# Kernel optimization log

Hardware: AMD Instinct MI355X
Metric: run time of the kernel (lower is better)

## Reference

```python
import jax, jax.numpy as jnp
import numpy as np

N = 50000      # nodes
E = 800000     # directed edges (avg degree 16)
IN, HID, OUT = 256, 128, 16


def setup_inputs() -> dict:
    key = jax.random.key(0)
    ks = jax.random.split(key, 8)
    x = jax.random.normal(ks[0], (N, IN), dtype=jnp.float32)
    edge_index = jax.random.randint(ks[1], (2, E), 0, N)
    W1 = jax.random.normal(ks[2], (IN, HID), dtype=jnp.float32) * (1.0 / np.sqrt(IN))
    b1 = jnp.zeros((HID,), jnp.float32)
    W2 = jax.random.normal(ks[3], (HID, HID), dtype=jnp.float32) * (1.0 / np.sqrt(HID))
    b2 = jnp.zeros((HID,), jnp.float32)
    Wc = jax.random.normal(ks[4], (HID, OUT), dtype=jnp.float32) * (1.0 / np.sqrt(HID))
    bc = jnp.zeros((OUT,), jnp.float32)
    return {"x": x, "W1": W1, "b1": b1, "W2": W2, "b2": b2,
            "Wc": Wc, "bc": bc, "edge_index": edge_index, "conv_time": 30}


def _gcn_norm(edge_index, n, dtype):
    # add self-loops, compute symmetric GCN normalization D^{-1/2}(A+I)D^{-1/2}
    loops = jnp.arange(n)
    src = jnp.concatenate([edge_index[0], loops])
    dst = jnp.concatenate([edge_index[1], loops])
    deg = jax.ops.segment_sum(jnp.ones_like(dst, dtype=dtype), dst, num_segments=n)
    dinv = jnp.where(deg > 0, jax.lax.rsqrt(deg), jnp.zeros_like(deg))
    norm = dinv[src] * dinv[dst]          # [E+N] edge weights
    return src, dst, norm


def _propagate(h, src, dst, norm, n, hops):
    # hops is a static Python int (conv_time)
    for _ in range(hops):
        h = jax.ops.segment_sum(h[src] * norm[:, None], dst, num_segments=n)
    return h


def reference(x, W1, b1, W2, b2, Wc, bc, edge_index, conv_time):
    n = x.shape[0]
    src, dst, norm = _gcn_norm(edge_index, n, x.dtype)
    # conv1: linear only (conv_time = 0)
    h = jax.nn.relu(x @ W1 + b1)
    # dropout is identity in eval mode
    # conv2: linear + conv_time hops of normalized propagation
    h = _propagate(h @ W2 + b2, src, dst, norm, n, int(conv_time))
    h = jax.nn.relu(h)
    # cls: linear + 1 hop
    h = _propagate(h @ Wc + bc, src, dst, norm, n, 1)
    return h
```

## Files before the change

### kernel.cpp

```cpp
#include <hip/hip_runtime.h>
#include <hip/hip_fp16.h>

#define NNODES 50000
#define NEDGES 800000
#define IN_F   256
#define HID_F  128
#define OUT_F  16
#define HOPS   30
#define MPAD   50048

typedef unsigned int u32;
typedef unsigned long long u64;
typedef _Float16 f16;
typedef f16 f16x8 __attribute__((ext_vector_type(8)));
typedef float f32x4 __attribute__((ext_vector_type(4)));
typedef u32 u32x4 __attribute__((ext_vector_type(4)));

union U32H2 { u32 u; __half2 h; };

__device__ inline float2 upk(u32 v) {
    U32H2 t; t.u = v;
    return __half22float2(t.h);
}
__device__ inline u32 pk2(float a, float b) {
    U32H2 t; t.h = __floats2half2_rn(a, b);
    return t.u;
}


__global__ void k_init_deg(int* __restrict__ deg, int n) {
    int i = blockIdx.x * blockDim.x + threadIdx.x;
    if (i < n) deg[i] = 1;
}

__global__ void k_count(const int* __restrict__ dst, int* __restrict__ deg, int e) {
    int i = blockIdx.x * blockDim.x + threadIdx.x;
    if (i < e) atomicAdd(&deg[dst[i]], 1);
}

__global__ void k_dinv(const int* __restrict__ deg, float* __restrict__ dinv, int n) {
    int i = blockIdx.x * blockDim.x + threadIdx.x;
    if (i < n) dinv[i] = rsqrtf((float)deg[i]);
}

__global__ void k_scan1(const int* __restrict__ deg, int* __restrict__ bsums, int n) {
    __shared__ int sh[256];
    int tid = threadIdx.x;
    int i = blockIdx.x * 256 + tid;
    sh[tid] = (i < n) ? deg[i] : 0;
    __syncthreads();
    for (int ofs = 128; ofs > 0; ofs >>= 1) {
        if (tid < ofs) sh[tid] += sh[tid + ofs];
        __syncthreads();
    }
    if (tid == 0) bsums[blockIdx.x] = sh[0];
}

__global__ void k_scan2(int* __restrict__ bsums, int nb, int* __restrict__ rp, int n) {
    if (threadIdx.x == 0 && blockIdx.x == 0) {
        int run = 0;
        for (int b = 0; b < nb; ++b) { int t = bsums[b]; bsums[b] = run; run += t; }
        rp[n] = run;
    }
}

__global__ void k_scan3(const int* __restrict__ deg, const int* __restrict__ bsums,
                        int* __restrict__ rp, int* __restrict__ cursor, int n) {
    __shared__ int sh[256];
    int tid = threadIdx.x;
    int i = blockIdx.x * 256 + tid;
    int v = (i < n) ? deg[i] : 0;
    sh[tid] = v;
    __syncthreads();
    for (int ofs = 1; ofs < 256; ofs <<= 1) {
        int t = 0;
        if (tid >= ofs) t = sh[tid - ofs];
        __syncthreads();
        sh[tid] += t;
        __syncthreads();
    }
    if (i < n) {
        int excl = sh[tid] - v + bsums[blockIdx.x];
        rp[i] = excl;
        cursor[i] = excl;
    }
}

__global__ void k_scatter(const int* __restrict__ src, const int* __restrict__ dst,
                          const float* __restrict__ dinv, int* __restrict__ cursor,
                          int2* __restrict__ ew, int e, int n) {
    int t = blockIdx.x * blockDim.x + threadIdx.x;
    if (t < e) {
        int s = src[t], d = dst[t];
        int pos = atomicAdd(&cursor[d], 1);
        ew[pos] = make_int2(s, __float_as_int(dinv[s] * dinv[d]));
    } else if (t < e + n) {
        int i = t - e;
        int pos = atomicAdd(&cursor[i], 1);
        float di = dinv[i];
        ew[pos] = make_int2(i, __float_as_int(di * di));
    }
}

__global__ void k_sortwave(const int* __restrict__ rp, int2* __restrict__ ew, int n) {
    int node = blockIdx.x * 4 + (threadIdx.x >> 6);
    int lane = threadIdx.x & 63;
    if (node >= n) return;
    int beg = rp[node], end = rp[node + 1];
    int deg = end - beg;
    if (deg > 64) return;
    int2 my = make_int2(0x7fffffff, 0);
    if (lane < deg) my = ew[beg + lane];
    int rank = 0;
    for (int k = 0; k < deg; ++k) {
        int sk = __shfl(my.x, k);
        rank += (sk < my.x) || (sk == my.x && k < lane);
    }
    if (lane < deg) ew[beg + rank] = my;
}

template<int K, int NC>
__global__ void k_cast_wt(const float* __restrict__ W, f16* __restrict__ Wt) {
    int i = blockIdx.x * blockDim.x + threadIdx.x;
    if (i < K * NC) {
        int k = i / NC, c = i % NC;
        Wt[(size_t)c * K + k] = (f16)W[i];
    }
}


template<int K, bool RELU, typename TA>
__global__ __launch_bounds__(256)
void k_gemm_mfma(const TA* __restrict__ A, const f16* __restrict__ Wt,
                 const float* __restrict__ b, f16* __restrict__ C, int M) {
    constexpr int KC = (K > 128) ? 128 : K;
    __shared__ f16 sa[64][KC + 8];
    __shared__ f16 sb[128][KC + 8];
    int tid  = threadIdx.x;
    int wid  = tid >> 6;
    int lane = tid & 63;
    int row0 = blockIdx.x * 64;
    int rowW = row0 + wid * 16;
    int rl   = lane & 15;
    int kc   = (lane >> 4) * 8;

    f32x4 acc[8];
#pragma unroll
    for (int n = 0; n < 8; ++n) acc[n] = (f32x4)0.f;

    int lr = wid * 16 + rl;

    for (int c = 0; c < K / KC; ++c) {
        int k0 = c * KC;
        if (c > 0) __syncthreads();
        if constexpr (sizeof(TA) == 4) {
            const float4* A4 = reinterpret_cast<const float4*>(A);
            constexpr int C4 = KC / 4;
            for (int idx = tid; idx < 64 * C4; idx += 256) {
                int r  = idx / C4;
                int c4 = idx % C4;
                int gr = row0 + r;
                if (gr >= M) gr = M - 1;
                float4 v = A4[(size_t)gr * (K / 4) + k0 / 4 + c4];
                f16 o[4] = {(f16)v.x, (f16)v.y, (f16)v.z, (f16)v.w};
                *reinterpret_cast<u64*>(&sa[r][c4 * 4]) = *reinterpret_cast<u64*>(o);
            }
        } else {
            const u32x4* A4 = reinterpret_cast<const u32x4*>(A);
            constexpr int C8 = KC / 8;
            for (int idx = tid; idx < 64 * C8; idx += 256) {
                int r  = idx / C8;
                int c8 = idx % C8;
                int gr = row0 + r;
                if (gr >= M) gr = M - 1;
                u32x4 v = A4[(size_t)gr * (K / 8) + k0 / 8 + c8];
                *reinterpret_cast<u32x4*>(&sa[r][c8 * 8]) = v;
            }
        }
        {
            const u32x4* B4 = reinterpret_cast<const u32x4*>(Wt);
            constexpr int C8 = KC / 8;
            for (int idx = tid; idx < 128 * C8; idx += 256) {
                int r  = idx / C8;
                int c8 = idx % C8;
                u32x4 v = B4[(size_t)r * (K / 8) + k0 / 8 + c8];
                *reinterpret_cast<u32x4*>(&sb[r][c8 * 8]) = v;
            }
        }
        __syncthreads();

#pragma unroll
        for (int kk = 0; kk < KC; kk += 32) {
            f16x8 aF = *reinterpret_cast<const f16x8*>(&sa[lr][kk + kc]);
#pragma unroll
            for (int n = 0; n < 8; ++n) {
                f16x8 bF = *reinterpret_cast<const f16x8*>(&sb[n * 16 + rl][kk + kc]);
                acc[n] = __builtin_amdgcn_mfma_f32_16x16x32_f16(aF, bF, acc[n], 0, 0, 0);
            }
        }
    }

#pragma unroll
    for (int n = 0; n < 8; ++n) {
        int col = n * 16 + rl;
        float bias = b[col];
#pragma unroll
        for (int j = 0; j < 4; ++j) {
            int row = rowW + 4 * (lane >> 4) + j;
            if (row < M) {
                float s = acc[n][j] + bias;
                if (RELU) s = fmaxf(s, 0.f);
                C[(size_t)row * 128 + col] = (f16)s;
            }
        }
    }
}


template<bool RELU>
__global__ void k_proph(const u32* __restrict__ Hin, u32* __restrict__ Hout,
                        const int* __restrict__ rp, const int2* __restrict__ ew,
                        int n) {
    int grp  = threadIdx.x >> 4;
    int lane = threadIdx.x & 15;
    int node = blockIdx.x * 16 + grp;
    if (node >= n) return;
    int beg = rp[node], end = rp[node + 1];
    const u32x4* H4 = reinterpret_cast<const u32x4*>(Hin);

    float acc[8];
#pragma unroll
    for (int i = 0; i < 8; ++i) acc[i] = 0.f;

    auto body = [&](int e) {
        int2 p   = ew[e];
        float ww = __int_as_float(p.y);
        u32x4 v  = H4[(size_t)p.x * 16 + lane];
#pragma unroll
        for (int q = 0; q < 4; ++q) {
            float2 f = upk(v[q]);
            acc[q * 2 + 0] += ww * f.x;
            acc[q * 2 + 1] += ww * f.y;
        }
    };

    int e = beg;
    for (; e + 1 < end; e += 2) { body(e); body(e + 1); }
    if (e < end) body(e);

    if (RELU) {
#pragma unroll
        for (int i = 0; i < 8; ++i) acc[i] = fmaxf(acc[i], 0.f);
    }
    u32x4 o;
#pragma unroll
    for (int q = 0; q < 4; ++q) o[q] = pk2(acc[q * 2], acc[q * 2 + 1]);
    reinterpret_cast<u32x4*>(Hout)[(size_t)node * 16 + lane] = o;
}


__global__ void k_cls_h(const u32* __restrict__ Ah, const float* __restrict__ Wc,
                        const float* __restrict__ bc, float* __restrict__ G, int M) {
    __shared__ float sa[64][132];
    __shared__ float4 sw4[512];
    int tid  = threadIdx.x;
    int row0 = blockIdx.x * 64;

    for (int idx = tid; idx < 512; idx += 256)
        sw4[idx] = reinterpret_cast<const float4*>(Wc)[idx];

    const uint4* A4 = reinterpret_cast<const uint4*>(Ah);
    for (int idx = tid; idx < 64 * 16; idx += 256) {
        int r = idx >> 4, c = idx & 15;
        int gr = row0 + r;
        uint4 v = (gr < M) ? A4[(size_t)gr * 16 + c]
                           : make_uint4(0u, 0u, 0u, 0u);
        float* dst = &sa[r][c * 8];
        const u32* vv = reinterpret_cast<const u32*>(&v);
#pragma unroll
        for (int q = 0; q < 4; ++q) {
            float2 f = upk(vv[q]);
            dst[q * 2 + 0] = f.x;
            dst[q * 2 + 1] = f.y;
        }
    }
    __syncthreads();

    int tc = tid & 3;
    int tr = tid >> 2;
    float4 acc = make_float4(0.f, 0.f, 0.f, 0.f);
    for (int k4 = 0; k4 < 32; ++k4) {
        float4 a = *reinterpret_cast<const float4*>(&sa[tr][k4 * 4]);
        const float* af = reinterpret_cast<const float*>(&a);
#pragma unroll
        for (int kk = 0; kk < 4; ++kk) {
            float4 wv = sw4[(k4 * 4 + kk) * 4 + tc];
            float av = af[kk];
            acc.x += av * wv.x; acc.y += av * wv.y;
            acc.z += av * wv.z; acc.w += av * wv.w;
        }
    }
    int r = row0 + tr;
    if (r < M) {
        float4 bb = reinterpret_cast<const float4*>(bc)[tc];
        acc.x += bb.x; acc.y += bb.y; acc.z += bb.z; acc.w += bb.w;
        reinterpret_cast<float4*>(G)[(size_t)r * 4 + tc] = acc;
    }
}


__global__ void k_prop16(const float* __restrict__ Gin, float* __restrict__ Out,
                         const int* __restrict__ rp, const int2* __restrict__ ew,
                         int n) {
    int g    = blockIdx.x * 64 + (threadIdx.x >> 2);
    int lane = threadIdx.x & 3;
    if (g >= n) return;
    int beg = rp[g], end = rp[g + 1];
    const float4* G4 = reinterpret_cast<const float4*>(Gin);
    float ax = 0.f, ay = 0.f, az = 0.f, aw = 0.f;
    for (int e = beg; e < end; ++e) {
        int2 p   = ew[e];
        float ww = __int_as_float(p.y);
        float4 hv = G4[(size_t)p.x * 4 + lane];
        ax += ww * hv.x; ay += ww * hv.y; az += ww * hv.z; aw += ww * hv.w;
    }
    reinterpret_cast<float4*>(Out)[(size_t)g * 4 + lane] = make_float4(ax, ay, az, aw);
}


extern "C" void kernel_launch(void* const* d_in, const int* in_sizes, int n_in,
                              void* d_out, int out_size, void* d_ws, size_t ws_size,
                              hipStream_t stream) {
    const float* x  = (const float*)d_in[0];
    const float* W1 = (const float*)d_in[1];
    const float* b1 = (const float*)d_in[2];
    const float* W2 = (const float*)d_in[3];
    const float* b2 = (const float*)d_in[4];
    const float* Wc = (const float*)d_in[5];
    const float* bc = (const float*)d_in[6];
    const int*   ei = (const int*)d_in[7];
    const int* srcp = ei;
    const int* dstp = ei + NEDGES;
    float* out = (float*)d_out;

    char* p = (char*)d_ws;
    auto alloc = [&](size_t bytes) -> char* {
        char* r = p;
        p += (bytes + 255) & ~(size_t)255;
        return r;
    };
    int*   deg    = (int*)  alloc(NNODES * 4);
    float* dinv   = (float*)alloc(NNODES * 4);
    int*   rp     = (int*)  alloc((NNODES + 1) * 4);
    int*   cursor = (int*)  alloc(NNODES * 4);
    int*   bsums  = (int*)  alloc(256 * 4);
    int2*  ew     = (int2*) alloc((size_t)(NEDGES + NNODES) * 8);
    f16*   W1t    = (f16*)  alloc((size_t)HID_F * IN_F * 2);
    f16*   W2t    = (f16*)  alloc((size_t)HID_F * HID_F * 2);
    f16*   H0h    = (f16*)  alloc((size_t)MPAD * HID_F * 2);
    u32*   Hh0    = (u32*)  alloc((size_t)MPAD * HID_F * 2);
    u32*   Hh1    = (u32*)  alloc((size_t)NNODES * HID_F * 2);
    float* G      = (float*)alloc((size_t)NNODES * OUT_F * 4);

    const int T = 256;
    auto nb = [](int n, int t) { return (n + t - 1) / t; };

    k_init_deg<<<nb(NNODES, T), T, 0, stream>>>(deg, NNODES);
    k_count<<<nb(NEDGES, T), T, 0, stream>>>(dstp, deg, NEDGES);
    k_dinv<<<nb(NNODES, T), T, 0, stream>>>(deg, dinv, NNODES);
    int NB = nb(NNODES, 256);
    k_scan1<<<NB, 256, 0, stream>>>(deg, bsums, NNODES);
    k_scan2<<<1, 1, 0, stream>>>(bsums, NB, rp, NNODES);
    k_scan3<<<NB, 256, 0, stream>>>(deg, bsums, rp, cursor, NNODES);
    k_scatter<<<nb(NEDGES + NNODES, T), T, 0, stream>>>(srcp, dstp, dinv, cursor,
                                                        ew, NEDGES, NNODES);
    k_sortwave<<<nb(NNODES, 4), 256, 0, stream>>>(rp, ew, NNODES);

    k_cast_wt<IN_F,  HID_F><<<nb(IN_F * HID_F, T), T, 0, stream>>>(W1, W1t);
    k_cast_wt<HID_F, HID_F><<<nb(HID_F * HID_F, T), T, 0, stream>>>(W2, W2t);

    int GB = MPAD / 64;
    k_gemm_mfma<IN_F,  true,  float><<<GB, 256, 0, stream>>>(x,   W1t, b1, H0h, NNODES);
    k_gemm_mfma<HID_F, false, f16  ><<<GB, 256, 0, stream>>>(H0h, W2t, b2, (f16*)Hh0, NNODES);

    u32* cur = Hh0;
    u32* nxt = Hh1;
    int PB = nb(NNODES, 16);
    for (int i = 0; i < HOPS; ++i) {
        if (i == HOPS - 1)
            k_proph<true ><<<PB, 256, 0, stream>>>(cur, nxt, rp, ew, NNODES);
        else
            k_proph<false><<<PB, 256, 0, stream>>>(cur, nxt, rp, ew, NNODES);
        u32* t = cur; cur = nxt; nxt = t;
    }

    k_cls_h<<<nb(NNODES, 64), 256, 0, stream>>>(cur, Wc, bc, G, NNODES);
    k_prop16<<<nb(NNODES, 64), 256, 0, stream>>>(G, out, rp, ew, NNODES);
}
```

Before: 1.076 ms.

## Fuse GEMMs with edge scatter and sort into shared launches

Merges the first GEMM with the CSR edge scatter, and the second GEMM with the per-node edge sort, into single kernels that split work by block index. The GEMM tile shrinks its K chunk to 64, issues all global loads into registers before writing shared memory, and sets a launch-bounds occupancy hint. The aim is to overlap independent preprocessing with GEMM work and cut launch count. In exchange, the heterogeneous blocks may compete for resources and the smaller K chunk adds more synchronisation steps.

Result: faster. 1.053 ms (-2.1%).

```diff
diff --git a/kernel.cpp b/kernel.cpp
--- a/kernel.cpp
+++ b/kernel.cpp
@@ -8,6 +8,7 @@
 #define OUT_F  16
 #define HOPS   30
 #define MPAD   50048
+#define GB_GEMM (MPAD / 64)
 
 typedef unsigned int u32;
 typedef unsigned long long u64;
@@ -86,39 +87,6 @@
     }
 }
 
-__global__ void k_scatter(const int* __restrict__ src, const int* __restrict__ dst,
-                          const float* __restrict__ dinv, int* __restrict__ cursor,
-                          int2* __restrict__ ew, int e, int n) {
-    int t = blockIdx.x * blockDim.x + threadIdx.x;
-    if (t < e) {
-        int s = src[t], d = dst[t];
-        int pos = atomicAdd(&cursor[d], 1);
-        ew[pos] = make_int2(s, __float_as_int(dinv[s] * dinv[d]));
-    } else if (t < e + n) {
-        int i = t - e;
-        int pos = atomicAdd(&cursor[i], 1);
-        float di = dinv[i];
-        ew[pos] = make_int2(i, __float_as_int(di * di));
-    }
-}
-
-__global__ void k_sortwave(const int* __restrict__ rp, int2* __restrict__ ew, int n) {
-    int node = blockIdx.x * 4 + (threadIdx.x >> 6);
-    int lane = threadIdx.x & 63;
-    if (node >= n) return;
-    int beg = rp[node], end = rp[node + 1];
-    int deg = end - beg;
-    if (deg > 64) return;
-    int2 my = make_int2(0x7fffffff, 0);
-    if (lane < deg) my = ew[beg + lane];
-    int rank = 0;
-    for (int k = 0; k < deg; ++k) {
-        int sk = __shfl(my.x, k);
-        rank += (sk < my.x) || (sk == my.x && k < lane);
-    }
-    if (lane < deg) ew[beg + rank] = my;
-}
-
 template<int K, int NC>
 __global__ void k_cast_wt(const float* __restrict__ W, f16* __restrict__ Wt) {
     int i = blockIdx.x * blockDim.x + threadIdx.x;
@@ -130,16 +98,16 @@
 
 
 template<int K, bool RELU, typename TA>
-__global__ __launch_bounds__(256)
-void k_gemm_mfma(const TA* __restrict__ A, const f16* __restrict__ Wt,
-                 const float* __restrict__ b, f16* __restrict__ C, int M) {
-    constexpr int KC = (K > 128) ? 128 : K;
+__device__ void gemm_tile(const TA* __restrict__ A, const f16* __restrict__ Wt,
+                          const float* __restrict__ b, f16* __restrict__ C,
+                          int M, int bid) {
+    constexpr int KC = 64;
     __shared__ f16 sa[64][KC + 8];
     __shared__ f16 sb[128][KC + 8];
     int tid  = threadIdx.x;
     int wid  = tid >> 6;
     int lane = tid & 63;
-    int row0 = blockIdx.x * 64;
+    int row0 = bid * 64;
     int rowW = row0 + wid * 16;
     int rl   = lane & 15;
     int kc   = (lane >> 4) * 8;
@@ -149,42 +117,71 @@
     for (int n = 0; n < 8; ++n) acc[n] = (f32x4)0.f;
 
     int lr = wid * 16 + rl;
+    const u32x4* B4 = reinterpret_cast<const u32x4*>(Wt);
 
     for (int c = 0; c < K / KC; ++c) {
         int k0 = c * KC;
         if (c > 0) __syncthreads();
         if constexpr (sizeof(TA) == 4) {
             const float4* A4 = reinterpret_cast<const float4*>(A);
-            constexpr int C4 = KC / 4;
-            for (int idx = tid; idx < 64 * C4; idx += 256) {
-                int r  = idx / C4;
-                int c4 = idx % C4;
+            float4 av[4];
+            u32x4  bv[4];
+#pragma unroll
+            for (int j = 0; j < 4; ++j) {
+                int idx = tid + j * 256;
+                int r = idx >> 4, c4 = idx & 15;
                 int gr = row0 + r;
                 if (gr >= M) gr = M - 1;
-                float4 v = A4[(size_t)gr * (K / 4) + k0 / 4 + c4];
-                f16 o[4] = {(f16)v.x, (f16)v.y, (f16)v.z, (f16)v.w};
+                av[j] = A4[(size_t)gr * (K / 4) + k0 / 4 + c4];
+            }
+#pragma unroll
+            for (int j = 0; j < 4; ++j) {
+                int idx = tid + j * 256;
+                int r = idx >> 3, c8 = idx & 7;
+                bv[j] = B4[(size_t)r * (K / 8) + k0 / 8 + c8];
+            }
+#pragma unroll
+            for (int j = 0; j < 4; ++j) {
+                int idx = tid + j * 256;
+                int r = idx >> 4, c4 = idx & 15;
+                f16 o[4] = {(f16)av[j].x, (f16)av[j].y, (f16)av[j].z, (f16)av[j].w};
                 *reinterpret_cast<u64*>(&sa[r][c4 * 4]) = *reinterpret_cast<u64*>(o);
+            }
+#pragma unroll
+            for (int j = 0; j < 4; ++j) {
+                int idx = tid + j * 256;
+                int r = idx >> 3, c8 = idx & 7;
+                *reinterpret_cast<u32x4*>(&sb[r][c8 * 8]) = bv[j];
             }
         } else {
             const u32x4* A4 = reinterpret_cast<const u32x4*>(A);
-            constexpr int C8 = KC / 8;
-            for (int idx = tid; idx < 64 * C8; idx += 256) {
-                int r  = idx / C8;
-                int c8 = idx % C8;
+            u32x4 av[2];
+            u32x4 bv[4];
+#pragma unroll
+            for (int j = 0; j < 2; ++j) {
+                int idx = tid + j * 256;
+                int r = idx >> 3, c8 = idx & 7;
                 int gr = row0 + r;
                 if (gr >= M) gr = M - 1;
-                u32x4 v = A4[(size_t)gr * (K / 8) + k0 / 8 + c8];
-                *reinterpret_cast<u32x4*>(&sa[r][c8 * 8]) = v;
-            }
-        }
-        {
-            const u32x4* B4 = reinterpret_cast<const u32x4*>(Wt);
-            constexpr int C8 = KC / 8;
-            for (int idx = tid; idx < 128 * C8; idx += 256) {
-                int r  = idx / C8;
-                int c8 = idx % C8;
-                u32x4 v = B4[(size_t)r * (K / 8) + k0 / 8 + c8];
-                *reinterpret_cast<u32x4*>(&sb[r][c8 * 8]) = v;
+                av[j] = A4[(size_t)gr * (K / 8) + k0 / 8 + c8];
+            }
+#pragma unroll
+            for (int j = 0; j < 4; ++j) {
+                int idx = tid + j * 256;
+                int r = idx >> 3, c8 = idx & 7;
+                bv[j] = B4[(size_t)r * (K / 8) + k0 / 8 + c8];
+            }
+#pragma unroll
+            for (int j = 0; j < 2; ++j) {
+                int idx = tid + j * 256;
+                int r = idx >> 3, c8 = idx & 7;
+                *reinterpret_cast<u32x4*>(&sa[r][c8 * 8]) = av[j];
+            }
+#pragma unroll
+            for (int j = 0; j < 4; ++j) {
+                int idx = tid + j * 256;
+                int r = idx >> 3, c8 = idx & 7;
+                *reinterpret_cast<u32x4*>(&sb[r][c8 * 8]) = bv[j];
             }
         }
         __syncthreads();
@@ -213,6 +210,55 @@
                 C[(size_t)row * 128 + col] = (f16)s;
             }
         }
+    }
+}
+
+
+__global__ __launch_bounds__(256, 4)
+void k_g1_scatter(const float* __restrict__ x, const f16* __restrict__ W1t,
+                  const float* __restrict__ b1, f16* __restrict__ H0h,
+                  const int* __restrict__ src, const int* __restrict__ dst,
+                  const float* __restrict__ dinv, int* __restrict__ cursor,
+                  int2* __restrict__ ew) {
+    if ((int)blockIdx.x < GB_GEMM) {
+        gemm_tile<IN_F, true, float>(x, W1t, b1, H0h, NNODES, blockIdx.x);
+    } else {
+        int t = (blockIdx.x - GB_GEMM) * 256 + threadIdx.x;
+        if (t < NEDGES) {
+            int s = src[t], d = dst[t];
+            int pos = atomicAdd(&cursor[d], 1);
+            ew[pos] = make_int2(s, __float_as_int(dinv[s] * dinv[d]));
+        } else if (t < NEDGES + NNODES) {
+            int i = t - NEDGES;
+            int pos = atomicAdd(&cursor[i], 1);
+            float di = dinv[i];
+            ew[pos] = make_int2(i, __float_as_int(di * di));
+        }
+    }
+}
+
+
+__global__ __launch_bounds__(256, 4)
+void k_g2_sort(const f16* __restrict__ H0h, const f16* __restrict__ W2t,
+               const float* __restrict__ b2, f16* __restrict__ Hh0,
+               const int* __restrict__ rp, int2* __restrict__ ew) {
+    if ((int)blockIdx.x < GB_GEMM) {
+        gemm_tile<HID_F, false, f16>(H0h, W2t, b2, Hh0, NNODES, blockIdx.x);
+    } else {
+        int node = (blockIdx.x - GB_GEMM) * 4 + (threadIdx.x >> 6);
+        int lane = threadIdx.x & 63;
+        if (node >= NNODES) return;
+        int beg = rp[node], end = rp[node + 1];
+        int deg = end - beg;
+        if (deg > 64) return;
+        int2 my = make_int2(0x7fffffff, 0);
+        if (lane < deg) my = ew[beg + lane];
+        int rank = 0;
+        for (int k = 0; k < deg; ++k) {
+            int sk = __shfl(my.x, k);
+            rank += (sk < my.x) || (sk == my.x && k < lane);
+        }
+        if (lane < deg) ew[beg + rank] = my;
     }
 }
 
@@ -372,16 +418,14 @@
     k_scan1<<<NB, 256, 0, stream>>>(deg, bsums, NNODES);
     k_scan2<<<1, 1, 0, stream>>>(bsums, NB, rp, NNODES);
     k_scan3<<<NB, 256, 0, stream>>>(deg, bsums, rp, cursor, NNODES);
-    k_scatter<<<nb(NEDGES + NNODES, T), T, 0, stream>>>(srcp, dstp, dinv, cursor,
-                                                        ew, NEDGES, NNODES);
-    k_sortwave<<<nb(NNODES, 4), 256, 0, stream>>>(rp, ew, NNODES);
-
     k_cast_wt<IN_F,  HID_F><<<nb(IN_F * HID_F, T), T, 0, stream>>>(W1, W1t);
     k_cast_wt<HID_F, HID_F><<<nb(HID_F * HID_F, T), T, 0, stream>>>(W2, W2t);
 
-    int GB = MPAD / 64;
-    k_gemm_mfma<IN_F,  true,  float><<<GB, 256, 0, stream>>>(x,   W1t, b1, H0h, NNODES);
-    k_gemm_mfma<HID_F, false, f16  ><<<GB, 256, 0, stream>>>(H0h, W2t, b2, (f16*)Hh0, NNODES);
+    int SCB = nb(NEDGES + NNODES, 256);
+    k_g1_scatter<<<GB_GEMM + SCB, 256, 0, stream>>>(x, W1t, b1, H0h,
+                                                    srcp, dstp, dinv, cursor, ew);
+    int SWB = nb(NNODES, 4);
+    k_g2_sort<<<GB_GEMM + SWB, 256, 0, stream>>>(H0h, W2t, b2, (f16*)Hh0, rp, ew);
 
     u32* cur = Hh0;
     u32* nxt = Hh1;
```
